# Kernel tuning notes

Hardware: AMD Instinct MI355X
Metric: run time of the kernel (lower is better)

Reference implementation:

```python
import jax, jax.numpy as jnp
import numpy as np

D_IN = 1024
D_OUT = 1024
NUM_HEADS = 16
HEAD_DIM = D_OUT // NUM_HEADS


def setup_inputs() -> dict:
    key = jax.random.key(0)
    ks = jax.random.split(key, 6)
    s = 0.02
    x = jax.random.normal(ks[0], (1, 4096, D_IN), dtype=jnp.float32)
    W_q = jax.random.normal(ks[1], (D_IN, D_OUT), dtype=jnp.float32) * s
    W_k = jax.random.normal(ks[2], (D_IN, D_OUT), dtype=jnp.float32) * s
    W_v = jax.random.normal(ks[3], (D_IN, D_OUT), dtype=jnp.float32) * s
    W_o = jax.random.normal(ks[4], (D_OUT, D_OUT), dtype=jnp.float32) * s
    b_o = jnp.zeros((D_OUT,), dtype=jnp.float32)
    return {"x": x, "W_q": W_q, "W_k": W_k, "W_v": W_v, "W_o": W_o, "b_o": b_o}


def reference(x, W_q, W_k, W_v, W_o, b_o):
    b, n, _ = x.shape
    # project and split heads: [b, h, n, d]
    def split_heads(t):
        return t.reshape(b, n, NUM_HEADS, HEAD_DIM).transpose(0, 2, 1, 3)
    q = split_heads(x @ W_q)
    k = split_heads(x @ W_k)
    v = split_heads(x @ W_v)
    scale = 1.0 / jnp.sqrt(jnp.float32(HEAD_DIM))
    scores = jnp.einsum('bhqd,bhkd->bhqk', q, k) * scale  # [b,h,n,n]
    causal = jnp.tril(jnp.ones((n, n), dtype=bool))
    scores = jnp.where(causal, scores, -jnp.inf)
    weights = jax.nn.softmax(scores, axis=-1)
    # dropout rate is 0.0 -> identity
    ctx = jnp.einsum('bhqk,bhkd->bhqd', weights, v)
    ctx = ctx.transpose(0, 2, 1, 3).reshape(b, n, D_OUT)
    return ctx @ W_o + b_o
```

## Files before the change

kernel.cpp:

```cpp
#include <hip/hip_runtime.h>
#include <hip/hip_bf16.h>

typedef __hip_bfloat16 bf16;
typedef __attribute__((ext_vector_type(8))) short short8;
typedef __attribute__((ext_vector_type(4))) short short4v;
typedef __attribute__((ext_vector_type(4))) float floatx4;

#define SEQ 4096
#define DIM 1024
#define NH 16
#define HD 64

__device__ __forceinline__ short f2s(float f) { bf16 t = __float2bfloat16(f); return *(short*)&t; }

__device__ __forceinline__ float fexp2(float x) {
#if __has_builtin(__builtin_amdgcn_exp2f)
    return __builtin_amdgcn_exp2f(x);
#else
    return exp2f(x);
#endif
}

__device__ __forceinline__ void gload16(const void* g, void* l) {
    __builtin_amdgcn_global_load_lds(
        (const __attribute__((address_space(1))) void*)g,
        (__attribute__((address_space(3))) void*)l, 16, 0, 0);
}

__device__ __forceinline__ short8 cvt8(float4 a, float4 b) {
    short8 s;
    s[0] = f2s(a.x); s[1] = f2s(a.y); s[2] = f2s(a.z); s[3] = f2s(a.w);
    s[4] = f2s(b.x); s[5] = f2s(b.y); s[6] = f2s(b.z); s[7] = f2s(b.w);
    return s;
}

__global__ __launch_bounds__(256) void transpose_cast_kernel(
    const float* __restrict__ W0, const float* __restrict__ W1,
    const float* __restrict__ W2, const float* __restrict__ W3,
    bf16* __restrict__ Wt_all)
{
    const float* W = blockIdx.z == 0 ? W0 : blockIdx.z == 1 ? W1
                   : blockIdx.z == 2 ? W2 : W3;
    bf16* Wt = Wt_all + (size_t)blockIdx.z * DIM * DIM;

    __shared__ float tile[32][33];
    const int n0 = blockIdx.x * 32, k0 = blockIdx.y * 32;
    const int tr = threadIdx.x >> 5;
    const int tc = threadIdx.x & 31;
#pragma unroll
    for (int i = 0; i < 32; i += 8)
        tile[tr + i][tc] = W[(size_t)(k0 + tr + i) * DIM + n0 + tc];
    __syncthreads();
#pragma unroll
    for (int i = 0; i < 32; i += 8)
        Wt[(size_t)(n0 + tr + i) * DIM + k0 + tc] = __float2bfloat16(tile[tc][tr + i]);
}

#define QBM 128
#define QBN 128
#define QBK 64
#define QSCALE 0.1803368801111244f

__global__ __launch_bounds__(256) void qkv_gemm_kernel(
    const float* __restrict__ A, const bf16* __restrict__ Wt,
    bf16* __restrict__ Qb, bf16* __restrict__ Kb, bf16* __restrict__ Vb)
{
    const int z = blockIdx.z;
    const bf16* Bt = Wt + (size_t)z * DIM * DIM;
    bf16* C = z == 0 ? Qb : (z == 1 ? Kb : Vb);
    const float osc = (z == 0) ? QSCALE : 1.0f;

    __shared__ alignas(16) float Af[QBM][QBK];
    __shared__ alignas(16) short Bs[QBN][QBK];

    const int tid  = threadIdx.x;
    const int wave = tid >> 6, lane = tid & 63;
    const int l15  = lane & 15, quad = lane >> 4;
    const int wm = (wave & 1) * 64;
    const int wn = (wave >> 1) * 64;
    const int bm = blockIdx.y * QBM;
    const int bn = blockIdx.x * QBN;

    const int arow = tid >> 4;
    const int agch = (tid & 15) ^ (arow & 15);
    const float* gA = A + (size_t)(bm + arow) * DIM + agch * 4;
    char* ldsA = (char*)&Af[0][0] + wave * 1024;

    const int brow = tid >> 3;
    const int bgch = (tid & 7) ^ (brow & 7);
    const bf16* gB = Bt + (size_t)(bn + brow) * DIM + bgch * 8;
    char* ldsB = (char*)&Bs[0][0] + wave * 1024;

    floatx4 acc[4][4] = {};

    for (int k0 = 0; k0 < DIM; k0 += QBK) {
        __syncthreads();
#pragma unroll
        for (int c = 0; c < 8; ++c)
            gload16(gA + (size_t)c * 16 * DIM + k0, ldsA + c * 4096);
#pragma unroll
        for (int c = 0; c < 4; ++c)
            gload16(gB + (size_t)c * 32 * DIM + k0, ldsB + c * 4096);
        __syncthreads();

#pragma unroll
        for (int c2 = 0; c2 < 2; ++c2) {
            const int g0 = c2 * 8 + quad * 2;
            const int cb = (c2 * 4 + quad) ^ (l15 & 7);
            short8 afr[4], bfr[4];
#pragma unroll
            for (int i = 0; i < 4; ++i) {
                const int ra = wm + i * 16 + l15;
                float4 f0 = *(const float4*)&Af[ra][(g0 ^ l15) * 4];
                float4 f1 = *(const float4*)&Af[ra][((g0 + 1) ^ l15) * 4];
                afr[i] = cvt8(f0, f1);
                bfr[i] = *(const short8*)&Bs[wn + i * 16 + l15][cb * 8];
            }
#pragma unroll
            for (int mi = 0; mi < 4; ++mi)
#pragma unroll
                for (int ni = 0; ni < 4; ++ni)
                    acc[mi][ni] = __builtin_amdgcn_mfma_f32_16x16x32_bf16(
                        afr[mi], bfr[ni], acc[mi][ni], 0, 0, 0);
        }
    }

#pragma unroll
    for (int mi = 0; mi < 4; ++mi)
#pragma unroll
        for (int r = 0; r < 4; ++r) {
            const int row = bm + wm + mi * 16 + quad * 4 + r;
#pragma unroll
            for (int ni = 0; ni < 4; ++ni) {
                const int col = bn + wn + ni * 16 + l15;
                C[(size_t)row * DIM + col] = __float2bfloat16(acc[mi][ni][r] * osc);
            }
        }
}

__global__ __launch_bounds__(256) void out_gemm_kernel(
    const bf16* __restrict__ A, const bf16* __restrict__ Bt,
    const float* __restrict__ bias, float* __restrict__ C)
{
    __shared__ alignas(16) short Asl[128][64];
    __shared__ alignas(16) short Bsl[64][64];

    const int tid  = threadIdx.x;
    const int wave = tid >> 6, lane = tid & 63;
    const int l15  = lane & 15, quad = lane >> 4;
    const int wm = (wave & 1) * 64;
    const int wn = (wave >> 1) * 32;
    const int bm = blockIdx.y * 128;
    const int bn = blockIdx.x * 64;

    const int srow   = tid >> 3;
    const int gchunk = (tid & 7) ^ (srow & 7);
    const bf16* gA = A  + (size_t)(bm + srow) * DIM + gchunk * 8;
    const bf16* gB = Bt + (size_t)(bn + srow) * DIM + gchunk * 8;
    char* ldsA = (char*)&Asl[0][0] + wave * 1024;
    char* ldsB = (char*)&Bsl[0][0] + wave * 1024;

    floatx4 acc[4][2] = {};

    for (int k0 = 0; k0 < DIM; k0 += 64) {
        __syncthreads();
#pragma unroll
        for (int c = 0; c < 4; ++c)
            gload16(gA + (size_t)c * 32 * DIM + k0, ldsA + c * 4096);
#pragma unroll
        for (int c = 0; c < 2; ++c)
            gload16(gB + (size_t)c * 32 * DIM + k0, ldsB + c * 4096);
        __syncthreads();

#pragma unroll
        for (int c2 = 0; c2 < 2; ++c2) {
            const int cb = (c2 * 4 + quad) ^ (l15 & 7);
            short8 afr[4], bfr[2];
#pragma unroll
            for (int i = 0; i < 4; ++i)
                afr[i] = *(const short8*)&Asl[wm + i * 16 + l15][cb * 8];
#pragma unroll
            for (int i = 0; i < 2; ++i)
                bfr[i] = *(const short8*)&Bsl[wn + i * 16 + l15][cb * 8];
#pragma unroll
            for (int mi = 0; mi < 4; ++mi)
#pragma unroll
                for (int ni = 0; ni < 2; ++ni)
                    acc[mi][ni] = __builtin_amdgcn_mfma_f32_16x16x32_bf16(
                        afr[mi], bfr[ni], acc[mi][ni], 0, 0, 0);
        }
    }

#pragma unroll
    for (int mi = 0; mi < 4; ++mi)
#pragma unroll
        for (int r = 0; r < 4; ++r) {
            const int row = bm + wm + mi * 16 + quad * 4 + r;
#pragma unroll
            for (int ni = 0; ni < 2; ++ni) {
                const int col = bn + wn + ni * 16 + l15;
                C[(size_t)row * DIM + col] = acc[mi][ni][r] + bias[col];
            }
        }
}

#define QT 128
#define KT 64

__global__ __launch_bounds__(256) void flash_attn_kernel(
    const bf16* __restrict__ Q, const bf16* __restrict__ K,
    const bf16* __restrict__ V, bf16* ctx)
{
    const int lin  = blockIdx.y * 32 + blockIdx.x;
    const int half = lin >> 8, idx = lin & 255;
    const int qj   = half ? (idx & 31) : 31 - (idx & 31);
    const int h    = (idx >> 5) + 8 * half;
    const int q0   = qj * QT;
    const int nkt  = 2 * qj + 2;

    const int tid  = threadIdx.x;
    const int wave = tid >> 6;
    const int lane = tid & 63;
    const int l15  = lane & 15;
    const int quad = lane >> 4;
    const int le   = l15 & 7;

    __shared__ alignas(16) short QP[128 * 64];
    __shared__ alignas(16) short Ks[2][64 * 64];
    __shared__ alignas(16) short Vt[2][64 * 64];

    {
        const int r = tid >> 1, e = r & 7;
        const short8* src = (const short8*)(Q + (size_t)(q0 + r) * DIM + h * HD + (tid & 1) * 32);
#pragma unroll
        for (int i = 0; i < 4; ++i) {
            const int c = (tid & 1) * 4 + i;
            *(short8*)&QP[r * 64 + ((c ^ e) * 8)] = src[i];
        }
    }

    const int kr = tid >> 2, ke = kr & 7, kc0 = (tid & 3) * 2;
    const int vw = tid & 31, vd = (tid >> 5) * 8, vr = vw * 2;

    {
        const short8* kp  = (const short8*)(K + (size_t)kr * DIM + h * HD + kc0 * 8);
        short8 k0r = kp[0], k1r = kp[1];
        const short8* vp0 = (const short8*)(V + (size_t)vr * DIM + h * HD + vd);
        const short8* vp1 = (const short8*)(V + (size_t)(vr + 1) * DIM + h * HD + vd);
        short8 v0r = vp0[0], v1r = vp1[0];
        *(short8*)&Ks[0][kr * 64 + ((kc0 ^ ke) * 8)]       = k0r;
        *(short8*)&Ks[0][kr * 64 + (((kc0 + 1) ^ ke) * 8)] = k1r;
#pragma unroll
        for (int i = 0; i < 8; ++i) {
            unsigned int pv = (unsigned int)(unsigned short)v0r[i]
                            | ((unsigned int)(unsigned short)v1r[i] << 16);
            const int row = vd + i;
            *(unsigned int*)&Vt[0][row * 64 + (((vw >> 2) ^ (row & 7)) * 8) + (vw & 3) * 2] = pv;
        }
    }

    short8 kreg[2][2], vreg[2][2];
    {
        const size_t nb = (size_t)KT;
        const short8* kp  = (const short8*)(K + (nb + kr) * DIM + h * HD + kc0 * 8);
        kreg[0][0] = kp[0]; kreg[0][1] = kp[1];
        const short8* vp0 = (const short8*)(V + (nb + vr) * DIM + h * HD + vd);
        const short8* vp1 = (const short8*)(V + (nb + vr + 1) * DIM + h * HD + vd);
        vreg[0][0] = vp0[0]; vreg[0][1] = vp1[0];
    }

    __syncthreads();

    short8 qfrag[2][2];
#pragma unroll
    for (int s = 0; s < 2; ++s)
#pragma unroll
        for (int c = 0; c < 2; ++c)
            qfrag[s][c] = *(const short8*)&QP[(wave * 32 + s * 16 + l15) * 64
                                              + (((c * 4 + quad) ^ le) * 8)];

    short8 onesf;
#pragma unroll
    for (int i = 0; i < 8; ++i) onesf[i] = (short)0x3F80;

    floatx4 o_acc[2][4] = {};
    floatx4 lacc[2] = {};
    const int prow = wave * 32 + l15;

    for (int kt2 = 0; kt2 < nkt; kt2 += 2) {
#pragma unroll
        for (int u = 0; u < 2; ++u) {
            const int kt = kt2 + u;

            if (kt + 2 < nkt) {
                const size_t nb = (size_t)(kt + 2) * KT;
                const short8* kp  = (const short8*)(K + (nb + kr) * DIM + h * HD + kc0 * 8);
                kreg[u ^ 1][0] = kp[0]; kreg[u ^ 1][1] = kp[1];
                const short8* vp0 = (const short8*)(V + (nb + vr) * DIM + h * HD + vd);
                const short8* vp1 = (const short8*)(V + (nb + vr + 1) * DIM + h * HD + vd);
                vreg[u ^ 1][0] = vp0[0]; vreg[u ^ 1][1] = vp1[0];
            }

            floatx4 sT[2][4] = {};
#pragma unroll
            for (int n = 0; n < 4; ++n)
#pragma unroll
                for (int c = 0; c < 2; ++c) {
                    short8 kf = *(const short8*)&Ks[u][(n * 16 + l15) * 64
                                                       + (((c * 4 + quad) ^ le) * 8)];
#pragma unroll
                    for (int s = 0; s < 2; ++s)
                        sT[s][n] = __builtin_amdgcn_mfma_f32_16x16x32_bf16(
                            kf, qfrag[s][c], sT[s][n], 0, 0, 0);
                }

            const int kbase = kt * KT;
            if (kt >= nkt - 2) {
#pragma unroll
                for (int s = 0; s < 2; ++s) {
                    const int qrow = q0 + wave * 32 + s * 16 + l15;
#pragma unroll
                    for (int n = 0; n < 4; ++n) {
                        const int key0 = kbase + n * 16 + quad * 4;
                        short4v pk;
#pragma unroll
                        for (int r = 0; r < 4; ++r)
                            pk[r] = f2s((key0 + r <= qrow) ? fexp2(sT[s][n][r]) : 0.f);
                        *(short4v*)&QP[(prow + s * 16) * 64
                                       + (((n * 2 + (quad >> 1)) ^ le) * 8) + (quad & 1) * 4] = pk;
                    }
                }
            } else {
#pragma unroll
                for (int s = 0; s < 2; ++s)
#pragma unroll
                    for (int n = 0; n < 4; ++n) {
                        short4v pk;
#pragma unroll
                        for (int r = 0; r < 4; ++r)
                            pk[r] = f2s(fexp2(sT[s][n][r]));
                        *(short4v*)&QP[(prow + s * 16) * 64
                                       + (((n * 2 + (quad >> 1)) ^ le) * 8) + (quad & 1) * 4] = pk;
                    }
            }

            short8 pfrag[2][2];
#pragma unroll
            for (int s = 0; s < 2; ++s)
#pragma unroll
                for (int c = 0; c < 2; ++c)
                    pfrag[s][c] = *(const short8*)&QP[(prow + s * 16) * 64
                                                      + (((c * 4 + quad) ^ le) * 8)];
#pragma unroll
            for (int n = 0; n < 4; ++n)
#pragma unroll
                for (int c = 0; c < 2; ++c) {
                    short8 vf = *(const short8*)&Vt[u][(n * 16 + l15) * 64
                                                       + (((c * 4 + quad) ^ le) * 8)];
#pragma unroll
                    for (int s = 0; s < 2; ++s)
                        o_acc[s][n] = __builtin_amdgcn_mfma_f32_16x16x32_bf16(
                            pfrag[s][c], vf, o_acc[s][n], 0, 0, 0);
                }
#pragma unroll
            for (int s = 0; s < 2; ++s) {
                lacc[s] = __builtin_amdgcn_mfma_f32_16x16x32_bf16(pfrag[s][0], onesf, lacc[s], 0, 0, 0);
                lacc[s] = __builtin_amdgcn_mfma_f32_16x16x32_bf16(pfrag[s][1], onesf, lacc[s], 0, 0, 0);
            }

            if (kt + 1 < nkt) {
                *(short8*)&Ks[u ^ 1][kr * 64 + ((kc0 ^ ke) * 8)]       = kreg[u][0];
                *(short8*)&Ks[u ^ 1][kr * 64 + (((kc0 + 1) ^ ke) * 8)] = kreg[u][1];
#pragma unroll
                for (int i = 0; i < 8; ++i) {
                    unsigned int pv = (unsigned int)(unsigned short)vreg[u][0][i]
                                    | ((unsigned int)(unsigned short)vreg[u][1][i] << 16);
                    const int row = vd + i;
                    *(unsigned int*)&Vt[u ^ 1][row * 64 + (((vw >> 2) ^ (row & 7)) * 8) + (vw & 3) * 2] = pv;
                }
            }
            __syncthreads();
        }
    }

#pragma unroll
    for (int s = 0; s < 2; ++s)
#pragma unroll
        for (int r = 0; r < 4; ++r) {
            const float inv = 1.0f / lacc[s][r];
            const int row = q0 + wave * 32 + s * 16 + quad * 4 + r;
#pragma unroll
            for (int n = 0; n < 4; ++n)
                ctx[(size_t)row * DIM + h * HD + n * 16 + l15] =
                    __float2bfloat16(o_acc[s][n][r] * inv);
        }
}

extern "C" void kernel_launch(void* const* d_in, const int* in_sizes, int n_in,
                              void* d_out, int out_size, void* d_ws, size_t ws_size,
                              hipStream_t stream)
{
    const float* x  = (const float*)d_in[0];
    const float* Wq = (const float*)d_in[1];
    const float* Wk = (const float*)d_in[2];
    const float* Wv = (const float*)d_in[3];
    const float* Wo = (const float*)d_in[4];
    const float* bo = (const float*)d_in[5];
    float* out = (float*)d_out;

    bf16* Wt_all = (bf16*)d_ws;
    bf16* Qb     = Wt_all + (size_t)4 * DIM * DIM;
    bf16* V      = (bf16*)d_out;
    bf16* Kb     = V + (size_t)SEQ * DIM;
    bf16* ctx    = Qb;
    const bf16* Wot = Wt_all + (size_t)3 * DIM * DIM;

    transpose_cast_kernel<<<dim3(32, 32, 4), 256, 0, stream>>>(Wq, Wk, Wv, Wo, Wt_all);

    qkv_gemm_kernel<<<dim3(DIM / QBN, SEQ / QBM, 3), 256, 0, stream>>>(
        x, Wt_all, Qb, Kb, V);

    flash_attn_kernel<<<dim3(32, NH), 256, 0, stream>>>(Qb, Kb, V, ctx);

    out_gemm_kernel<<<dim3(DIM / 64, SEQ / 128), 256, 0, stream>>>(
        ctx, Wot, bo, out);
}
```

Measured before the change: 200.4 us.

## Split causal attention KV range across two blocks, merge partials, remap GEMM grids

```diff
diff --git a/kernel.cpp b/kernel.cpp
--- a/kernel.cpp
+++ b/kernel.cpp
@@ -12,6 +12,7 @@
 #define HD 64
 
 __device__ __forceinline__ short f2s(float f) { bf16 t = __float2bfloat16(f); return *(short*)&t; }
+__device__ __forceinline__ float s2f(short s) { bf16 t = *(bf16*)&s; return __bfloat162float(t); }
 
 __device__ __forceinline__ float fexp2(float x) {
 #if __has_builtin(__builtin_amdgcn_exp2f)
@@ -65,7 +66,13 @@
     const float* __restrict__ A, const bf16* __restrict__ Wt,
     bf16* __restrict__ Qb, bf16* __restrict__ Kb, bf16* __restrict__ Vb)
 {
-    const int z = blockIdx.z;
+    const int lin = blockIdx.x;
+    const int xcd = lin & 7, i5 = lin >> 3;
+    const int bm = (xcd * 4 + (i5 & 3)) * QBM;
+    const int rest = i5 >> 2;
+    const int bn = (rest & 7) * QBN;
+    const int z = rest >> 3;
+
     const bf16* Bt = Wt + (size_t)z * DIM * DIM;
     bf16* C = z == 0 ? Qb : (z == 1 ? Kb : Vb);
     const float osc = (z == 0) ? QSCALE : 1.0f;
@@ -78,8 +85,6 @@
     const int l15  = lane & 15, quad = lane >> 4;
     const int wm = (wave & 1) * 64;
     const int wn = (wave >> 1) * 64;
-    const int bm = blockIdx.y * QBM;
-    const int bn = blockIdx.x * QBN;
 
     const int arow = tid >> 4;
     const int agch = (tid & 15) ^ (arow & 15);
@@ -142,6 +147,11 @@
     const bf16* __restrict__ A, const bf16* __restrict__ Bt,
     const float* __restrict__ bias, float* __restrict__ C)
 {
+    const int lin = blockIdx.x;
+    const int xcd = lin & 7, i5 = lin >> 3;
+    const int bm = (xcd * 4 + (i5 & 3)) * 128;
+    const int bn = (i5 >> 2) * 64;
+
     __shared__ alignas(16) short Asl[128][64];
     __shared__ alignas(16) short Bsl[64][64];
 
@@ -150,8 +160,6 @@
     const int l15  = lane & 15, quad = lane >> 4;
     const int wm = (wave & 1) * 64;
     const int wn = (wave >> 1) * 32;
-    const int bm = blockIdx.y * 128;
-    const int bn = blockIdx.x * 64;
 
     const int srow   = tid >> 3;
     const int gchunk = (tid & 7) ^ (srow & 7);
@@ -204,19 +212,22 @@
         }
 }
 
-#define QT 128
+#define QT 256
 #define KT 64
 
-__global__ __launch_bounds__(256) void flash_attn_kernel(
+__global__ __launch_bounds__(512, 4) void flash_attn_kernel(
     const bf16* __restrict__ Q, const bf16* __restrict__ K,
-    const bf16* __restrict__ V, bf16* ctx)
-{
-    const int lin  = blockIdx.y * 32 + blockIdx.x;
-    const int half = lin >> 8, idx = lin & 255;
-    const int qj   = half ? (idx & 31) : 31 - (idx & 31);
-    const int h    = (idx >> 5) + 8 * half;
+    const bf16* __restrict__ V, bf16* __restrict__ pO, float* __restrict__ pl)
+{
+    const int lin  = blockIdx.x;
+    const int idx  = lin & 255;
+    const int half = lin >> 8;
+    const int h    = idx >> 4, t = idx & 15;
+    const int qj   = half ? t : 15 - t;
     const int q0   = qj * QT;
-    const int nkt  = 2 * qj + 2;
+    const int nktF = 4 * qj + 4;
+    const int ktS  = half ? (nktF >> 1) : 0;
+    const int ktE  = half ? nktF : (nktF >> 1);
 
     const int tid  = threadIdx.x;
     const int wave = tid >> 6;
@@ -225,7 +236,7 @@
     const int quad = lane >> 4;
     const int le   = l15 & 7;
 
-    __shared__ alignas(16) short QP[128 * 64];
+    __shared__ alignas(16) short QP[256 * 64];
     __shared__ alignas(16) short Ks[2][64 * 64];
     __shared__ alignas(16) short Vt[2][64 * 64];
 
@@ -239,34 +250,30 @@
         }
     }
 
-    const int kr = tid >> 2, ke = kr & 7, kc0 = (tid & 3) * 2;
-    const int vw = tid & 31, vd = (tid >> 5) * 8, vr = vw * 2;
+    const int kr = tid >> 3, ke = kr & 7, kc = tid & 7;
+    const int vp = tid & 31, vg = (tid >> 5) * 4;
+    const int vr = vp * 2;
 
     {
-        const short8* kp  = (const short8*)(K + (size_t)kr * DIM + h * HD + kc0 * 8);
-        short8 k0r = kp[0], k1r = kp[1];
-        const short8* vp0 = (const short8*)(V + (size_t)vr * DIM + h * HD + vd);
-        const short8* vp1 = (const short8*)(V + (size_t)(vr + 1) * DIM + h * HD + vd);
-        short8 v0r = vp0[0], v1r = vp1[0];
-        *(short8*)&Ks[0][kr * 64 + ((kc0 ^ ke) * 8)]       = k0r;
-        *(short8*)&Ks[0][kr * 64 + (((kc0 + 1) ^ ke) * 8)] = k1r;
-#pragma unroll
-        for (int i = 0; i < 8; ++i) {
-            unsigned int pv = (unsigned int)(unsigned short)v0r[i]
-                            | ((unsigned int)(unsigned short)v1r[i] << 16);
-            const int row = vd + i;
-            *(unsigned int*)&Vt[0][row * 64 + (((vw >> 2) ^ (row & 7)) * 8) + (vw & 3) * 2] = pv;
-        }
-    }
-
-    short8 kreg[2][2], vreg[2][2];
+        short8 k0r = *(const short8*)(K + (size_t)(ktS * KT + kr) * DIM + h * HD + kc * 8);
+        short4v va = *(const short4v*)(V + (size_t)(ktS * KT + vr) * DIM + h * HD + vg);
+        short4v vb = *(const short4v*)(V + (size_t)(ktS * KT + vr + 1) * DIM + h * HD + vg);
+        *(short8*)&Ks[0][kr * 64 + ((kc ^ ke) * 8)] = k0r;
+#pragma unroll
+        for (int i = 0; i < 4; ++i) {
+            unsigned int pv = (unsigned int)(unsigned short)va[i]
+                            | ((unsigned int)(unsigned short)vb[i] << 16);
+            const int d = vg + i;
+            *(unsigned int*)&Vt[0][d * 64 + (((vp >> 2) ^ (d & 7)) * 8) + (vp & 3) * 2] = pv;
+        }
+    }
+    short8 kreg[2];
+    short4v vrga[2], vrgb[2];
     {
-        const size_t nb = (size_t)KT;
-        const short8* kp  = (const short8*)(K + (nb + kr) * DIM + h * HD + kc0 * 8);
-        kreg[0][0] = kp[0]; kreg[0][1] = kp[1];
-        const short8* vp0 = (const short8*)(V + (nb + vr) * DIM + h * HD + vd);
-        const short8* vp1 = (const short8*)(V + (nb + vr + 1) * DIM + h * HD + vd);
-        vreg[0][0] = vp0[0]; vreg[0][1] = vp1[0];
+        const size_t nb = (size_t)(ktS + 1) * KT;
+        kreg[0] = *(const short8*)(K + (nb + kr) * DIM + h * HD + kc * 8);
+        vrga[0] = *(const short4v*)(V + (nb + vr) * DIM + h * HD + vg);
+        vrgb[0] = *(const short4v*)(V + (nb + vr + 1) * DIM + h * HD + vg);
     }
 
     __syncthreads();
@@ -287,18 +294,16 @@
     floatx4 lacc[2] = {};
     const int prow = wave * 32 + l15;
 
-    for (int kt2 = 0; kt2 < nkt; kt2 += 2) {
+    for (int kt2 = ktS; kt2 < ktE; kt2 += 2) {
 #pragma unroll
         for (int u = 0; u < 2; ++u) {
             const int kt = kt2 + u;
 
-            if (kt + 2 < nkt) {
+            if (kt + 2 < ktE) {
                 const size_t nb = (size_t)(kt + 2) * KT;
-                const short8* kp  = (const short8*)(K + (nb + kr) * DIM + h * HD + kc0 * 8);
-                kreg[u ^ 1][0] = kp[0]; kreg[u ^ 1][1] = kp[1];
-                const short8* vp0 = (const short8*)(V + (nb + vr) * DIM + h * HD + vd);
-                const short8* vp1 = (const short8*)(V + (nb + vr + 1) * DIM + h * HD + vd);
-                vreg[u ^ 1][0] = vp0[0]; vreg[u ^ 1][1] = vp1[0];
+                kreg[u ^ 1] = *(const short8*)(K + (nb + kr) * DIM + h * HD + kc * 8);
+                vrga[u ^ 1] = *(const short4v*)(V + (nb + vr) * DIM + h * HD + vg);
+                vrgb[u ^ 1] = *(const short4v*)(V + (nb + vr + 1) * DIM + h * HD + vg);
             }
 
             floatx4 sT[2][4] = {};
@@ -314,14 +319,13 @@
                             kf, qfrag[s][c], sT[s][n], 0, 0, 0);
                 }
 
-            const int kbase = kt * KT;
-            if (kt >= nkt - 2) {
+            if (kt >= nktF - 4) {
 #pragma unroll
                 for (int s = 0; s < 2; ++s) {
                     const int qrow = q0 + wave * 32 + s * 16 + l15;
 #pragma unroll
                     for (int n = 0; n < 4; ++n) {
-                        const int key0 = kbase + n * 16 + quad * 4;
+                        const int key0 = kt * KT + n * 16 + quad * 4;
                         short4v pk;
 #pragma unroll
                         for (int r = 0; r < 4; ++r)
@@ -368,32 +372,49 @@
                 lacc[s] = __builtin_amdgcn_mfma_f32_16x16x32_bf16(pfrag[s][1], onesf, lacc[s], 0, 0, 0);
             }
 
-            if (kt + 1 < nkt) {
-                *(short8*)&Ks[u ^ 1][kr * 64 + ((kc0 ^ ke) * 8)]       = kreg[u][0];
-                *(short8*)&Ks[u ^ 1][kr * 64 + (((kc0 + 1) ^ ke) * 8)] = kreg[u][1];
-#pragma unroll
-                for (int i = 0; i < 8; ++i) {
-                    unsigned int pv = (unsigned int)(unsigned short)vreg[u][0][i]
-                                    | ((unsigned int)(unsigned short)vreg[u][1][i] << 16);
-                    const int row = vd + i;
-                    *(unsigned int*)&Vt[u ^ 1][row * 64 + (((vw >> 2) ^ (row & 7)) * 8) + (vw & 3) * 2] = pv;
+            if (kt + 1 < ktE) {
+                *(short8*)&Ks[u ^ 1][kr * 64 + ((kc ^ ke) * 8)] = kreg[u];
+#pragma unroll
+                for (int i = 0; i < 4; ++i) {
+                    unsigned int pv = (unsigned int)(unsigned short)vrga[u][i]
+                                    | ((unsigned int)(unsigned short)vrgb[u][i] << 16);
+                    const int d = vg + i;
+                    *(unsigned int*)&Vt[u ^ 1][d * 64 + (((vp >> 2) ^ (d & 7)) * 8) + (vp & 3) * 2] = pv;
                 }
             }
             __syncthreads();
         }
     }
 
+    bf16* pOh = pO + (size_t)half * SEQ * DIM;
+    float* plh = pl + (size_t)half * SEQ * NH;
 #pragma unroll
     for (int s = 0; s < 2; ++s)
 #pragma unroll
         for (int r = 0; r < 4; ++r) {
-            const float inv = 1.0f / lacc[s][r];
             const int row = q0 + wave * 32 + s * 16 + quad * 4 + r;
 #pragma unroll
             for (int n = 0; n < 4; ++n)
-                ctx[(size_t)row * DIM + h * HD + n * 16 + l15] =
-                    __float2bfloat16(o_acc[s][n][r] * inv);
-        }
+                pOh[(size_t)row * DIM + h * HD + n * 16 + l15] =
+                    __float2bfloat16(o_acc[s][n][r]);
+            if (l15 == 0) plh[(size_t)row * NH + h] = lacc[s][r];
+        }
+}
+
+__global__ __launch_bounds__(256) void merge_kernel(
+    const bf16* __restrict__ pO, const float* __restrict__ pl,
+    bf16* __restrict__ ctx)
+{
+    const int idx = (blockIdx.x * 256 + threadIdx.x) * 8;
+    const int row = idx >> 10, col = idx & 1023, h = col >> 6;
+    short8 a = *(const short8*)(pO + idx);
+    short8 b = *(const short8*)(pO + (size_t)SEQ * DIM + idx);
+    const float inv = 1.0f / (pl[(size_t)row * NH + h] + pl[(size_t)SEQ * NH + row * NH + h]);
+    short8 o;
+#pragma unroll
+    for (int i = 0; i < 8; ++i)
+        o[i] = f2s((s2f(a[i]) + s2f(b[i])) * inv);
+    *(short8*)(ctx + idx) = o;
 }
 
 extern "C" void kernel_launch(void* const* d_in, const int* in_sizes, int n_in,
@@ -408,20 +429,22 @@
     const float* bo = (const float*)d_in[5];
     float* out = (float*)d_out;
 
-    bf16* Wt_all = (bf16*)d_ws;
-    bf16* Qb     = Wt_all + (size_t)4 * DIM * DIM;
-    bf16* V      = (bf16*)d_out;
-    bf16* Kb     = V + (size_t)SEQ * DIM;
-    bf16* ctx    = Qb;
+    bf16*  Wt_all = (bf16*)d_ws;
+    bf16*  Qb     = Wt_all + (size_t)4 * DIM * DIM;
+    bf16*  V      = (bf16*)d_out;
+    bf16*  Kb     = V + (size_t)SEQ * DIM;
+    bf16*  ctx    = Qb;
+    bf16*  pO     = (bf16*)d_in[0];
+    float* pl     = (float*)d_ws;
     const bf16* Wot = Wt_all + (size_t)3 * DIM * DIM;
 
     transpose_cast_kernel<<<dim3(32, 32, 4), 256, 0, stream>>>(Wq, Wk, Wv, Wo, Wt_all);
 
-    qkv_gemm_kernel<<<dim3(DIM / QBN, SEQ / QBM, 3), 256, 0, stream>>>(
-        x, Wt_all, Qb, Kb, V);
-
-    flash_attn_kernel<<<dim3(32, NH), 256, 0, stream>>>(Qb, Kb, V, ctx);
-
-    out_gemm_kernel<<<dim3(DIM / 64, SEQ / 128), 256, 0, stream>>>(
-        ctx, Wot, bo, out);
-}
+    qkv_gemm_kernel<<<dim3(768), 256, 0, stream>>>(x, Wt_all, Qb, Kb, V);
+
+    flash_attn_kernel<<<dim3(512), 512, 0, stream>>>(Qb, Kb, V, pO, pl);
+
+    merge_kernel<<<dim3(SEQ * DIM / 2048), 256, 0, stream>>>(pO, pl, ctx);
+
+    out_gemm_kernel<<<dim3(512), 256, 0, stream>>>(ctx, Wot, bo, out);
+}
```

After: 273.0 us. 1.36x slower.
